# Kernel tuning notes

Hardware: AMD Instinct MI355X
Metric: run time of the kernel (lower is better)

Reference implementation:

```python
import jax, jax.numpy as jnp
import numpy as np
from jax import lax

C_IN, N_BR, K, H, W_IMG, B = 16, 32, 5, 224, 224, 16
C_SEL = C_IN // 2  # each pattern column selects exactly 8 channels
# circulant connectivity pattern, matches init_kwargs pattern literal
PATTERN = ((np.arange(C_IN)[:, None] + np.arange(N_BR)[None, :]) % C_IN < C_SEL).astype(np.int64)
# np.where returns sorted indices, matching the torch forward's index order
IDX = np.stack([np.where(PATTERN[:, i] == 1)[0] for i in range(N_BR)])  # [N_BR, C_SEL]


def setup_inputs() -> dict:
    key = jax.random.key(0)
    k1, k2, k3 = jax.random.split(key, 3)
    x = jax.random.normal(k1, (B, C_IN, H, W_IMG), dtype=jnp.float32)
    # per-branch conv weights stacked: branch i has Conv2d(8 -> 1, 5x5)
    Wc = jax.random.normal(k2, (N_BR, C_SEL, K, K), dtype=jnp.float32) * 0.05
    bc = jax.random.normal(k3, (N_BR,), dtype=jnp.float32) * 0.05
    return {"x": x, "Wc": Wc, "bc": bc}


def reference(x, Wc, bc):
    # gather the selected channels for every branch: [B, N_BR*C_SEL, H, W]
    x_sel = x[:, IDX.reshape(-1)]
    # all branches at once as a grouped convolution (groups = N_BR, 1 out/group)
    y = lax.conv_general_dilated(
        x_sel, Wc,
        window_strides=(1, 1),
        padding=[(2, 2), (2, 2)],
        feature_group_count=N_BR,
        dimension_numbers=("NCHW", "OIHW", "NCHW"),
    )  # [B, N_BR, H, W]
    return jax.nn.sigmoid(y + bc[None, :, None, None])
```

## Files before the change

### kernel.cpp

```cpp
#include <hip/hip_runtime.h>
#include <math.h>


#define HH 224
#define WW 224
#define BB 16
#define CIN 16
#define NBR 32
#define KSTEPS 13
#define LROWS 6
#define LCOLS 228

typedef short short8 __attribute__((ext_vector_type(8)));
typedef float f32x4 __attribute__((ext_vector_type(4)));

static __device__ __forceinline__ unsigned short f2bf(float f) {
    unsigned int u = __float_as_uint(f);
    unsigned int r = (u + 0x7FFFu + ((u >> 16) & 1u)) >> 16;
    return (unsigned short)r;
}

__global__ __launch_bounds__(64)
void prep_wfrag(const float* __restrict__ Wc, short* __restrict__ ws) {
    int t = blockIdx.x * 64 + threadIdx.x;
    int lane = t & 63;
    int rest = t >> 6;
    int nt = rest & 1;
    int kstep = rest >> 1;
    int n = lane & 15;
    int bi = nt * 16 + n;
    int kbase = kstep * 32 + (lane >> 4) * 8;
    short v[8];
    #pragma unroll
    for (int j = 0; j < 8; ++j) {
        int kg = kbase + j;
        float val = 0.0f;
        if (kg < 400) {
            int tap = kg >> 4;
            int c = kg & 15;
            if (((c + bi) & 15) < 8) {
                int jsel = 0;
                for (int cc = 0; cc < c; ++cc) jsel += (((cc + bi) & 15) < 8) ? 1 : 0;
                val = Wc[(bi * 8 + jsel) * 25 + tap];
            }
        }
        v[j] = (short)f2bf(val);
    }
    short8 pack;
    #pragma unroll
    for (int j = 0; j < 8; ++j) pack[j] = v[j];
    *(short8*)(ws + (size_t)t * 8) = pack;
}

__global__ __launch_bounds__(448)
void semiconv_mfma(const float* __restrict__ x,
                   const short* __restrict__ wfrag,
                   const float* __restrict__ bc,
                   float* __restrict__ out) {
    __shared__ short tile[LROWS * LCOLS * CIN];

    const int bidx = blockIdx.x;
    const int b = blockIdx.y;
    const int h = (bidx & 7) * 28 + (bidx >> 3);
    const int tid = threadIdx.x;

    for (int idx = tid; idx < LROWS * LCOLS; idx += 448) {
        int row = idx / LCOLS;
        int col = idx - row * LCOLS;
        int gh = h + row - 2;
        int gw = col - 2;
        unsigned int pk[8];
        if (row < 5 && (unsigned)gh < HH && (unsigned)gw < WW) {
            const float* xp = x + ((size_t)b * CIN * HH + gh) * WW + gw;
            #pragma unroll
            for (int cc = 0; cc < 8; ++cc) {
                float f0 = xp[(size_t)(2 * cc    ) * (HH * WW)];
                float f1 = xp[(size_t)(2 * cc + 1) * (HH * WW)];
                pk[cc] = (unsigned)f2bf(f0) | ((unsigned)f2bf(f1) << 16);
            }
        } else {
            #pragma unroll
            for (int cc = 0; cc < 8; ++cc) pk[cc] = 0;
        }
        int4* dst = (int4*)&tile[idx * CIN];
        dst[0] = make_int4(pk[0], pk[1], pk[2], pk[3]);
        dst[1] = make_int4(pk[4], pk[5], pk[6], pk[7]);
    }
    __syncthreads();

    const int wave = tid >> 6;
    const int lane = tid & 63;
    const int m = lane & 15;
    const int c0 = ((lane >> 4) & 1) * 8;
    const int half = lane >> 5;
    const int wbase = wave * 32;
    const int baseIdx = (wbase + m) * CIN + c0;

    f32x4 acc[2][2] = {};
    const short8* wfv = (const short8*)wfrag;

    #pragma unroll
    for (int k = 0; k < KSTEPS; ++k) {
        const int tapA = 2 * k, tapB = 2 * k + 1;
        const int offA = ((tapA / 5) * LCOLS + (tapA % 5)) * CIN;
        const int offB = ((tapB / 5) * LCOLS + (tapB % 5)) * CIN;
        const int tapoff = half ? offB : offA;
        short8 b0 = wfv[(k * 2 + 0) * 64 + lane];
        short8 b1 = wfv[(k * 2 + 1) * 64 + lane];
        #pragma unroll
        for (int mt = 0; mt < 2; ++mt) {
            short8 a = *(const short8*)&tile[tapoff + baseIdx + mt * 16 * CIN];
            acc[mt][0] = __builtin_amdgcn_mfma_f32_16x16x32_bf16(a, b0, acc[mt][0], 0, 0, 0);
            acc[mt][1] = __builtin_amdgcn_mfma_f32_16x16x32_bf16(a, b1, acc[mt][1], 0, 0, 0);
        }
    }

    const int rowm = (lane >> 4) * 4;
    #pragma unroll
    for (int nt = 0; nt < 2; ++nt) {
        const int branch = nt * 16 + m;
        const float bias = bc[branch];
        #pragma unroll
        for (int mt = 0; mt < 2; ++mt) {
            #pragma unroll
            for (int r = 0; r < 4; ++r) {
                const int w = wbase + mt * 16 + rowm + r;
                float s = acc[mt][nt][r] + bias;
                float sg = 1.0f / (1.0f + __expf(-s));
                out[(((size_t)b * NBR + branch) * HH + h) * WW + w] = sg;
            }
        }
    }
}

extern "C" void kernel_launch(void* const* d_in, const int* in_sizes, int n_in,
                              void* d_out, int out_size, void* d_ws, size_t ws_size,
                              hipStream_t stream) {
    const float* x  = (const float*)d_in[0];
    const float* Wc = (const float*)d_in[1];
    const float* bc = (const float*)d_in[2];
    float* out = (float*)d_out;
    short* wfrag = (short*)d_ws;

    prep_wfrag<<<26, 64, 0, stream>>>(Wc, wfrag);
    dim3 grid(224, 16);
    semiconv_mfma<<<grid, 448, 0, stream>>>(x, wfrag, bc, out);
}
```

Measured before the change: 180.1 us.

## Pre-transpose input to padded bf16 NHWC and stage tiles via global_load_lds

Adds a separate kernel that converts x once into a zero-padded bf16 channel-last buffer. The main kernel then copies its 5-row tile straight into LDS with global_load_lds, instead of each block re-reading five rows of strided fp32 with scalar loads and converting them. The epilogue now writes float4 vectors and uses a fast reciprocal for the sigmoid. The cost is an extra launch plus a round trip through an intermediate buffer in workspace.

```diff
diff --git a/kernel.cpp b/kernel.cpp
--- a/kernel.cpp
+++ b/kernel.cpp
@@ -7,17 +7,16 @@
 #define BB 16
 #define CIN 16
 #define NBR 32
+#define PH 228
+#define PW 228
 #define KSTEPS 13
-#define LROWS 6
-#define LCOLS 228
 
 typedef short short8 __attribute__((ext_vector_type(8)));
 typedef float f32x4 __attribute__((ext_vector_type(4)));
 
 static __device__ __forceinline__ unsigned short f2bf(float f) {
     unsigned int u = __float_as_uint(f);
-    unsigned int r = (u + 0x7FFFu + ((u >> 16) & 1u)) >> 16;
-    return (unsigned short)r;
+    return (unsigned short)((u + 0x7FFFu + ((u >> 16) & 1u)) >> 16);
 }
 
 __global__ __launch_bounds__(64)
@@ -30,7 +29,7 @@
     int n = lane & 15;
     int bi = nt * 16 + n;
     int kbase = kstep * 32 + (lane >> 4) * 8;
-    short v[8];
+    short8 pack;
     #pragma unroll
     for (int j = 0; j < 8; ++j) {
         int kg = kbase + j;
@@ -44,72 +43,104 @@
                 val = Wc[(bi * 8 + jsel) * 25 + tap];
             }
         }
-        v[j] = (short)f2bf(val);
+        pack[j] = (short)f2bf(val);
     }
-    short8 pack;
-    #pragma unroll
-    for (int j = 0; j < 8; ++j) pack[j] = v[j];
     *(short8*)(ws + (size_t)t * 8) = pack;
 }
 
+__global__ __launch_bounds__(256)
+void transpose_x(const float* __restrict__ x, short* __restrict__ xT) {
+    const int b = blockIdx.y;
+    const int prow = blockIdx.x * 4 + (threadIdx.x >> 6);
+    const int t = threadIdx.x & 63;
+    const int gh = prow - 2;
+    short* dst = xT + ((size_t)b * PH + prow) * (PW * CIN);
+
+    if (t < 56) {
+        const int gw = t * 4;
+        unsigned int pk[4][8];
+        if ((unsigned)gh < HH) {
+            const float* xp = x + (size_t)b * CIN * HH * WW + (size_t)gh * WW + gw;
+            #pragma unroll
+            for (int w2 = 0; w2 < 8; ++w2) {
+                float4 v0 = *(const float4*)(xp + (size_t)(2 * w2) * (HH * WW));
+                float4 v1 = *(const float4*)(xp + (size_t)(2 * w2 + 1) * (HH * WW));
+                const float* f0 = (const float*)&v0;
+                const float* f1 = (const float*)&v1;
+                #pragma unroll
+                for (int p = 0; p < 4; ++p)
+                    pk[p][w2] = (unsigned)f2bf(f0[p]) | ((unsigned)f2bf(f1[p]) << 16);
+            }
+        } else {
+            #pragma unroll
+            for (int p = 0; p < 4; ++p)
+                #pragma unroll
+                for (int w2 = 0; w2 < 8; ++w2) pk[p][w2] = 0u;
+        }
+        #pragma unroll
+        for (int p = 0; p < 4; ++p) {
+            int4* o = (int4*)(dst + (size_t)(gw + 2 + p) * CIN);
+            o[0] = make_int4(pk[p][0], pk[p][1], pk[p][2], pk[p][3]);
+            o[1] = make_int4(pk[p][4], pk[p][5], pk[p][6], pk[p][7]);
+        }
+    } else if (t == 56) {
+        int4 z = make_int4(0, 0, 0, 0);
+        int4* o0 = (int4*)(dst);
+        o0[0] = z; o0[1] = z;
+        int4* o1 = (int4*)(dst + 226 * CIN);
+        o1[0] = z; o1[1] = z;
+    }
+}
+
 __global__ __launch_bounds__(448)
-void semiconv_mfma(const float* __restrict__ x,
+void semiconv_main(const short* __restrict__ xT,
                    const short* __restrict__ wfrag,
                    const float* __restrict__ bc,
                    float* __restrict__ out) {
-    __shared__ short tile[LROWS * LCOLS * CIN];
+    __shared__ short tile[5 * PW * CIN];
 
     const int bidx = blockIdx.x;
     const int b = blockIdx.y;
     const int h = (bidx & 7) * 28 + (bidx >> 3);
     const int tid = threadIdx.x;
+    const int wave = tid >> 6;
+    const int lane = tid & 63;
 
-    for (int idx = tid; idx < LROWS * LCOLS; idx += 448) {
-        int row = idx / LCOLS;
-        int col = idx - row * LCOLS;
-        int gh = h + row - 2;
-        int gw = col - 2;
-        unsigned int pk[8];
-        if (row < 5 && (unsigned)gh < HH && (unsigned)gw < WW) {
-            const float* xp = x + ((size_t)b * CIN * HH + gh) * WW + gw;
-            #pragma unroll
-            for (int cc = 0; cc < 8; ++cc) {
-                float f0 = xp[(size_t)(2 * cc    ) * (HH * WW)];
-                float f1 = xp[(size_t)(2 * cc + 1) * (HH * WW)];
-                pk[cc] = (unsigned)f2bf(f0) | ((unsigned)f2bf(f1) << 16);
-            }
-        } else {
-            #pragma unroll
-            for (int cc = 0; cc < 8; ++cc) pk[cc] = 0;
-        }
-        int4* dst = (int4*)&tile[idx * CIN];
-        dst[0] = make_int4(pk[0], pk[1], pk[2], pk[3]);
-        dst[1] = make_int4(pk[4], pk[5], pk[6], pk[7]);
+    const short* src0 = xT + ((size_t)b * PH + h) * (PW * CIN);
+    #pragma unroll
+    for (int i = 0; i < 5; ++i) {
+        __builtin_amdgcn_global_load_lds(
+            (const __attribute__((address_space(1))) void*)(src0 + (size_t)(tid + i * 448) * 8),
+            (__attribute__((address_space(3))) void*)(tile + (wave * 64 + i * 448) * 8),
+            16, 0, 0);
+    }
+    if (tid < 40) {
+        const int chunk = 2240 + tid;
+        *(int4*)(tile + chunk * 8) = *(const int4*)(src0 + (size_t)chunk * 8);
     }
     __syncthreads();
 
-    const int wave = tid >> 6;
-    const int lane = tid & 63;
     const int m = lane & 15;
     const int c0 = ((lane >> 4) & 1) * 8;
     const int half = lane >> 5;
     const int wbase = wave * 32;
-    const int baseIdx = (wbase + m) * CIN + c0;
+    const int baseA = (wbase + m) * CIN + c0;
 
     f32x4 acc[2][2] = {};
     const short8* wfv = (const short8*)wfrag;
 
     #pragma unroll
     for (int k = 0; k < KSTEPS; ++k) {
-        const int tapA = 2 * k, tapB = 2 * k + 1;
-        const int offA = ((tapA / 5) * LCOLS + (tapA % 5)) * CIN;
-        const int offB = ((tapB / 5) * LCOLS + (tapB % 5)) * CIN;
+        const int tA = 2 * k, tB = 2 * k + 1;
+        const int offA = (tA / 5) * (PW * CIN) + (tA % 5) * CIN;
+        const int offB = (tB < 25) ? (tB / 5) * (PW * CIN) + (tB % 5) * CIN
+                                   : offA;
         const int tapoff = half ? offB : offA;
         short8 b0 = wfv[(k * 2 + 0) * 64 + lane];
         short8 b1 = wfv[(k * 2 + 1) * 64 + lane];
         #pragma unroll
         for (int mt = 0; mt < 2; ++mt) {
-            short8 a = *(const short8*)&tile[tapoff + baseIdx + mt * 16 * CIN];
+            short8 a = *(const short8*)&tile[tapoff + baseA + mt * 16 * CIN];
             acc[mt][0] = __builtin_amdgcn_mfma_f32_16x16x32_bf16(a, b0, acc[mt][0], 0, 0, 0);
             acc[mt][1] = __builtin_amdgcn_mfma_f32_16x16x32_bf16(a, b1, acc[mt][1], 0, 0, 0);
         }
@@ -122,13 +153,13 @@
         const float bias = bc[branch];
         #pragma unroll
         for (int mt = 0; mt < 2; ++mt) {
-            #pragma unroll
-            for (int r = 0; r < 4; ++r) {
-                const int w = wbase + mt * 16 + rowm + r;
-                float s = acc[mt][nt][r] + bias;
-                float sg = 1.0f / (1.0f + __expf(-s));
-                out[(((size_t)b * NBR + branch) * HH + h) * WW + w] = sg;
-            }
+            const int w = wbase + mt * 16 + rowm;
+            float4 v;
+            v.x = __builtin_amdgcn_rcpf(1.0f + __expf(-(acc[mt][nt][0] + bias)));
+            v.y = __builtin_amdgcn_rcpf(1.0f + __expf(-(acc[mt][nt][1] + bias)));
+            v.z = __builtin_amdgcn_rcpf(1.0f + __expf(-(acc[mt][nt][2] + bias)));
+            v.w = __builtin_amdgcn_rcpf(1.0f + __expf(-(acc[mt][nt][3] + bias)));
+            *(float4*)(out + (((size_t)b * NBR + branch) * HH + h) * WW + w) = v;
         }
     }
 }
@@ -140,9 +171,11 @@
     const float* Wc = (const float*)d_in[1];
     const float* bc = (const float*)d_in[2];
     float* out = (float*)d_out;
+
     short* wfrag = (short*)d_ws;
+    short* xT    = (short*)((char*)d_ws + 32768);
 
     prep_wfrag<<<26, 64, 0, stream>>>(Wc, wfrag);
-    dim3 grid(224, 16);
-    semiconv_mfma<<<grid, 448, 0, stream>>>(x, wfrag, bc, out);
+    transpose_x<<<dim3(57, 16), 256, 0, stream>>>(x, xT);
+    semiconv_main<<<dim3(224, 16), 448, 0, stream>>>(xT, wfrag, bc, out);
 }
```

Result: no change. 182.6 us (+1.4%).

## Process 7-row bands per block with a rolling LDS ring and prefetch

Applied to the files above, without the earlier changes.

Each block now handles a band of 7 output rows and keeps a 6-slot ring of staged input rows in shared memory. The next input row is loaded into registers while the current row is computed, so each input row is read about once per band instead of five times. Weight fragments are held in registers for the whole band, and the LDS layout is swizzled to avoid bank conflicts. Outputs are written as float4 stores using a fast reciprocal sigmoid. The grid shrinks to 512 blocks, which may lower parallelism, and the heavy register use risks reducing occupancy.

```diff
diff --git a/kernel.cpp b/kernel.cpp
--- a/kernel.cpp
+++ b/kernel.cpp
@@ -4,20 +4,20 @@
 
 #define HH 224
 #define WW 224
-#define BB 16
 #define CIN 16
 #define NBR 32
+#define HW (HH * WW)
 #define KSTEPS 13
-#define LROWS 6
-#define LCOLS 228
+#define RROWS 7
+#define RING 6
+#define UNITS 456
 
 typedef short short8 __attribute__((ext_vector_type(8)));
 typedef float f32x4 __attribute__((ext_vector_type(4)));
 
 static __device__ __forceinline__ unsigned short f2bf(float f) {
     unsigned int u = __float_as_uint(f);
-    unsigned int r = (u + 0x7FFFu + ((u >> 16) & 1u)) >> 16;
-    return (unsigned short)r;
+    return (unsigned short)((u + 0x7FFFu + ((u >> 16) & 1u)) >> 16);
 }
 
 __global__ __launch_bounds__(64)
@@ -30,7 +30,7 @@
     int n = lane & 15;
     int bi = nt * 16 + n;
     int kbase = kstep * 32 + (lane >> 4) * 8;
-    short v[8];
+    short8 pack;
     #pragma unroll
     for (int j = 0; j < 8; ++j) {
         int kg = kbase + j;
@@ -44,93 +44,124 @@
                 val = Wc[(bi * 8 + jsel) * 25 + tap];
             }
         }
-        v[j] = (short)f2bf(val);
+        pack[j] = (short)f2bf(val);
     }
-    short8 pack;
-    #pragma unroll
-    for (int j = 0; j < 8; ++j) pack[j] = v[j];
     *(short8*)(ws + (size_t)t * 8) = pack;
 }
 
-__global__ __launch_bounds__(448)
-void semiconv_mfma(const float* __restrict__ x,
-                   const short* __restrict__ wfrag,
-                   const float* __restrict__ bc,
-                   float* __restrict__ out) {
-    __shared__ short tile[LROWS * LCOLS * CIN];
+__global__ __launch_bounds__(512, 6)
+void semiconv_fused(const float* __restrict__ x,
+                    const short* __restrict__ wfrag,
+                    const float* __restrict__ bc,
+                    float* __restrict__ out) {
+    __shared__ short ring[RING * UNITS * 8];
 
-    const int bidx = blockIdx.x;
-    const int b = blockIdx.y;
-    const int h = (bidx & 7) * 28 + (bidx >> 3);
-    const int tid = threadIdx.x;
-
-    for (int idx = tid; idx < LROWS * LCOLS; idx += 448) {
-        int row = idx / LCOLS;
-        int col = idx - row * LCOLS;
-        int gh = h + row - 2;
-        int gw = col - 2;
-        unsigned int pk[8];
-        if (row < 5 && (unsigned)gh < HH && (unsigned)gw < WW) {
-            const float* xp = x + ((size_t)b * CIN * HH + gh) * WW + gw;
-            #pragma unroll
-            for (int cc = 0; cc < 8; ++cc) {
-                float f0 = xp[(size_t)(2 * cc    ) * (HH * WW)];
-                float f1 = xp[(size_t)(2 * cc + 1) * (HH * WW)];
-                pk[cc] = (unsigned)f2bf(f0) | ((unsigned)f2bf(f1) << 16);
-            }
-        } else {
-            #pragma unroll
-            for (int cc = 0; cc < 8; ++cc) pk[cc] = 0;
-        }
-        int4* dst = (int4*)&tile[idx * CIN];
-        dst[0] = make_int4(pk[0], pk[1], pk[2], pk[3]);
-        dst[1] = make_int4(pk[4], pk[5], pk[6], pk[7]);
-    }
-    __syncthreads();
-
+    const int band = blockIdx.x;
+    const int b    = blockIdx.y;
+    const int h0   = band * RROWS;
+    const int tid  = threadIdx.x;
     const int wave = tid >> 6;
     const int lane = tid & 63;
-    const int m = lane & 15;
-    const int c0 = ((lane >> 4) & 1) * 8;
-    const int half = lane >> 5;
+
+    const bool stg = tid < 2 * 228;
+    const int  spx = tid >> 1;
+    const int  sh8 = tid & 1;
+    const int  sgw = spx - 2;
+    const bool gwok = (unsigned)sgw < (unsigned)WW;
+    const float* xs = x + ((size_t)(b * CIN + sh8 * 8) * HH) * WW + (gwok ? sgw : 0);
+    const int  sunit = spx * 2 + (sh8 ^ ((spx >> 2) & 1));
+
+    float v[8];
+
+#define LD_ROW(pr) do {                                                   \
+        int gh_ = (pr) - 2;                                               \
+        bool rok_ = (unsigned)gh_ < (unsigned)HH;                         \
+        const float* xp_ = xs + (size_t)(rok_ ? gh_ : 0) * WW;            \
+        bool ok_ = rok_ && gwok;                                          \
+        _Pragma("unroll")                                                 \
+        for (int i_ = 0; i_ < 8; ++i_) {                                  \
+            float t_ = xp_[(size_t)i_ * HW];                              \
+            v[i_] = ok_ ? t_ : 0.0f;                                      \
+        }                                                                 \
+    } while (0)
+
+#define WR_ROW(pr) do {                                                   \
+        int slot_ = (pr) % RING;                                          \
+        int4 pk_;                                                         \
+        pk_.x = (int)((unsigned)f2bf(v[0]) | ((unsigned)f2bf(v[1]) << 16)); \
+        pk_.y = (int)((unsigned)f2bf(v[2]) | ((unsigned)f2bf(v[3]) << 16)); \
+        pk_.z = (int)((unsigned)f2bf(v[4]) | ((unsigned)f2bf(v[5]) << 16)); \
+        pk_.w = (int)((unsigned)f2bf(v[6]) | ((unsigned)f2bf(v[7]) << 16)); \
+        *(int4*)&ring[(slot_ * UNITS + sunit) * 8] = pk_;                 \
+    } while (0)
+
+    const int m     = lane & 15;
+    const int chalf = (lane >> 4) & 1;
+    const int half  = lane >> 5;
     const int wbase = wave * 32;
-    const int baseIdx = (wbase + m) * CIN + c0;
+    const int pxm   = wbase + m;
 
-    f32x4 acc[2][2] = {};
-    const short8* wfv = (const short8*)wfrag;
+    short8 bf[2 * KSTEPS];
+    #pragma unroll
+    for (int i = 0; i < 2 * KSTEPS; ++i)
+        bf[i] = ((const short8*)wfrag)[i * 64 + lane];
 
-    #pragma unroll
-    for (int k = 0; k < KSTEPS; ++k) {
-        const int tapA = 2 * k, tapB = 2 * k + 1;
-        const int offA = ((tapA / 5) * LCOLS + (tapA % 5)) * CIN;
-        const int offB = ((tapB / 5) * LCOLS + (tapB % 5)) * CIN;
-        const int tapoff = half ? offB : offA;
-        short8 b0 = wfv[(k * 2 + 0) * 64 + lane];
-        short8 b1 = wfv[(k * 2 + 1) * 64 + lane];
-        #pragma unroll
-        for (int mt = 0; mt < 2; ++mt) {
-            short8 a = *(const short8*)&tile[tapoff + baseIdx + mt * 16 * CIN];
-            acc[mt][0] = __builtin_amdgcn_mfma_f32_16x16x32_bf16(a, b0, acc[mt][0], 0, 0, 0);
-            acc[mt][1] = __builtin_amdgcn_mfma_f32_16x16x32_bf16(a, b1, acc[mt][1], 0, 0, 0);
-        }
+    #pragma unroll 1
+    for (int p = 0; p < 4; ++p) {
+        if (stg) { LD_ROW(h0 + p); WR_ROW(h0 + p); }
     }
+    if (stg) LD_ROW(h0 + 4);
 
-    const int rowm = (lane >> 4) * 4;
-    #pragma unroll
-    for (int nt = 0; nt < 2; ++nt) {
-        const int branch = nt * 16 + m;
-        const float bias = bc[branch];
-        #pragma unroll
-        for (int mt = 0; mt < 2; ++mt) {
+    #pragma unroll 1
+    for (int r = 0; r < RROWS; ++r) {
+        if (stg) WR_ROW(h0 + 4 + r);
+        __syncthreads();
+        if (stg && r < RROWS - 1) LD_ROW(h0 + 5 + r);
+
+        if (wave < 7) {
+            int slv[5];
             #pragma unroll
-            for (int r = 0; r < 4; ++r) {
-                const int w = wbase + mt * 16 + rowm + r;
-                float s = acc[mt][nt][r] + bias;
-                float sg = 1.0f / (1.0f + __expf(-s));
-                out[(((size_t)b * NBR + branch) * HH + h) * WW + w] = sg;
+            for (int kh = 0; kh < 5; ++kh) slv[kh] = (h0 + r + kh) % RING;
+
+            f32x4 acc[2][2] = {};
+            #pragma unroll
+            for (int s = 0; s < KSTEPS; ++s) {
+                const int tap0 = 2 * s;
+                const int tap1 = (2 * s + 1 < 25) ? (2 * s + 1) : 24;
+                const int kh0 = tap0 / 5, kw0 = tap0 % 5;
+                const int kh1 = tap1 / 5, kw1 = tap1 % 5;
+                const int sl = half ? slv[kh1] : slv[kh0];
+                const int px = pxm + (half ? kw1 : kw0);
+                const int u0 = (sl * UNITS + px * 2 + (chalf ^ ((px >> 2) & 1))) * 8;
+                const short8 a0 = *(const short8*)&ring[u0];
+                const short8 a1 = *(const short8*)&ring[u0 + 256];
+                acc[0][0] = __builtin_amdgcn_mfma_f32_16x16x32_bf16(a0, bf[2*s],   acc[0][0], 0, 0, 0);
+                acc[0][1] = __builtin_amdgcn_mfma_f32_16x16x32_bf16(a0, bf[2*s+1], acc[0][1], 0, 0, 0);
+                acc[1][0] = __builtin_amdgcn_mfma_f32_16x16x32_bf16(a1, bf[2*s],   acc[1][0], 0, 0, 0);
+                acc[1][1] = __builtin_amdgcn_mfma_f32_16x16x32_bf16(a1, bf[2*s+1], acc[1][1], 0, 0, 0);
+            }
+
+            const int hrow = h0 + r;
+            const int rowm = (lane >> 4) * 4;
+            #pragma unroll
+            for (int nt = 0; nt < 2; ++nt) {
+                const int branch = nt * 16 + m;
+                const float bias = bc[branch];
+                #pragma unroll
+                for (int mt = 0; mt < 2; ++mt) {
+                    const int w0c = wbase + mt * 16 + rowm;
+                    float4 o;
+                    o.x = __builtin_amdgcn_rcpf(1.0f + __expf(-(acc[mt][nt][0] + bias)));
+                    o.y = __builtin_amdgcn_rcpf(1.0f + __expf(-(acc[mt][nt][1] + bias)));
+                    o.z = __builtin_amdgcn_rcpf(1.0f + __expf(-(acc[mt][nt][2] + bias)));
+                    o.w = __builtin_amdgcn_rcpf(1.0f + __expf(-(acc[mt][nt][3] + bias)));
+                    *(float4*)(out + (((size_t)b * NBR + branch) * HH + hrow) * WW + w0c) = o;
+                }
             }
         }
     }
+#undef LD_ROW
+#undef WR_ROW
 }
 
 extern "C" void kernel_launch(void* const* d_in, const int* in_sizes, int n_in,
@@ -143,6 +174,5 @@
     short* wfrag = (short*)d_ws;
 
     prep_wfrag<<<26, 64, 0, stream>>>(Wc, wfrag);
-    dim3 grid(224, 16);
-    semiconv_mfma<<<grid, 448, 0, stream>>>(x, wfrag, bc, out);
+    semiconv_fused<<<dim3(32, 16), 512, 0, stream>>>(x, wfrag, bc, out);
 }
```

After: 279.5 us. 1.55x slower.
